# Performance work log

Measured on AMD Instinct MI355X. Metric: run time of the kernel, lower is better.

## Reference

```python
import jax, jax.numpy as jnp
import numpy as np

N, E, F_IN, HID, HEADS, NT, B = 50000, 400000, 32, 64, 4, 20, 64
IN1 = F_IN + HID  # 96, conv1 input dim after concat with node-type embedding


def _glorot(key, shape):
    fan_in = shape[0]
    return jax.random.normal(key, shape, dtype=jnp.float32) / np.sqrt(fan_in)


def setup_inputs() -> dict:
    key = jax.random.key(0)
    ks = jax.random.split(key, 40)
    inp = {
        "x": jax.random.normal(ks[0], (N, F_IN), dtype=jnp.float32),
        "edge_index": jax.random.randint(ks[1], (2, E), 0, N, dtype=jnp.int32),
        "edge_attr": jax.random.normal(ks[2], (E,), dtype=jnp.float32),
        "batch": jnp.sort(jax.random.randint(ks[3], (N,), 0, B, dtype=jnp.int32)),
        "node_type": jax.random.randint(ks[4], (N,), 0, NT, dtype=jnp.int32),
        # parameters
        "node_emb": jax.random.normal(ks[5], (NT, HID), dtype=jnp.float32) * 0.1,
        "edge_W": _glorot(ks[6], (1, HID)), "edge_b": jnp.zeros((HID,), jnp.float32),
        # GATConv 1 (in=96, out=64, heads=4, edge_dim=64, concat=False)
        "W1": _glorot(ks[7], (IN1, HEADS * HID)),
        "att_src1": jax.random.normal(ks[8], (HEADS, HID), jnp.float32) * 0.1,
        "att_dst1": jax.random.normal(ks[9], (HEADS, HID), jnp.float32) * 0.1,
        "We1": _glorot(ks[10], (HID, HEADS * HID)),
        "att_e1": jax.random.normal(ks[11], (HEADS, HID), jnp.float32) * 0.1,
        "b1": jnp.zeros((HID,), jnp.float32),
        # GATConv 2 (in=64)
        "W2": _glorot(ks[12], (HID, HEADS * HID)),
        "att_src2": jax.random.normal(ks[13], (HEADS, HID), jnp.float32) * 0.1,
        "att_dst2": jax.random.normal(ks[14], (HEADS, HID), jnp.float32) * 0.1,
        "We2": _glorot(ks[15], (HID, HEADS * HID)),
        "att_e2": jax.random.normal(ks[16], (HEADS, HID), jnp.float32) * 0.1,
        "b2": jnp.zeros((HID,), jnp.float32),
        # SAGEConv (mean aggr): out = mean_agg @ Wl + x @ Wr + b
        "sage_Wl": _glorot(ks[17], (HID, HID)), "sage_Wr": _glorot(ks[18], (HID, HID)),
        "sage_b": jnp.zeros((HID,), jnp.float32),
        "lin1_W": _glorot(ks[19], (HID, HID)), "lin1_b": jnp.zeros((HID,), jnp.float32),
        "lin2_W": _glorot(ks[20], (HID, HID)), "lin2_b": jnp.zeros((HID,), jnp.float32),
        "tel_W": _glorot(ks[21], (HID, 1)), "tel_b": jnp.zeros((1,), jnp.float32),
        "comp_W": _glorot(ks[22], (HID, 1)), "comp_b": jnp.zeros((1,), jnp.float32),
        "pch_W": _glorot(ks[23], (HID, 1)), "pch_b": jnp.zeros((1,), jnp.float32),
    }
    return inp


def _gat(x, src, dst, edge_h, W, att_s, att_d, We, att_e, b):
    n = x.shape[0]
    h = (x @ W).reshape(n, HEADS, HID)                       # [N,H,C]
    a_s = (h * att_s).sum(-1)                                # [N,H]
    a_d = (h * att_d).sum(-1)
    e = (edge_h @ We).reshape(-1, HEADS, HID)                # [E,H,C]
    a_e = (e * att_e).sum(-1)                                # [E,H]
    alpha = jax.nn.leaky_relu(a_s[src] + a_d[dst] + a_e, 0.2)
    m = jax.ops.segment_max(alpha, dst, num_segments=n)
    m = jnp.where(jnp.isfinite(m), m, 0.0)
    ex = jnp.exp(alpha - m[dst])
    den = jax.ops.segment_sum(ex, dst, num_segments=n)
    alpha = ex / (den[dst] + 1e-16)                          # segment softmax per dst
    out = jax.ops.segment_sum(h[src] * alpha[..., None], dst, num_segments=n)
    return out.mean(axis=1) + b                              # concat=False -> head mean


def reference(x, edge_index, edge_attr, batch, node_type, node_emb, edge_W, edge_b,
              W1, att_src1, att_dst1, We1, att_e1, b1,
              W2, att_src2, att_dst2, We2, att_e2, b2,
              sage_Wl, sage_Wr, sage_b, lin1_W, lin1_b, lin2_W, lin2_b,
              tel_W, tel_b, comp_W, comp_b, pch_W, pch_b):
    src, dst = edge_index[0], edge_index[1]
    edge_h = edge_attr[:, None] @ edge_W + edge_b            # [E,HID]
    h = jnp.concatenate([x, node_emb[node_type]], axis=-1)   # [N,96]
    h = jax.nn.elu(_gat(h, src, dst, edge_h, W1, att_src1, att_dst1, We1, att_e1, b1))
    h = jax.nn.elu(_gat(h, src, dst, edge_h, W2, att_src2, att_dst2, We2, att_e2, b2))
    # SAGEConv with mean aggregation
    deg = jax.ops.segment_sum(jnp.ones((src.shape[0],), h.dtype), dst, num_segments=N)
    agg = jax.ops.segment_sum(h[src], dst, num_segments=N) / jnp.maximum(deg, 1.0)[:, None]
    h = jax.nn.elu(agg @ sage_Wl + h @ sage_Wr + sage_b)
    # global mean pool over graphs
    cnt = jax.ops.segment_sum(jnp.ones((N,), h.dtype), batch, num_segments=B)
    g = jax.ops.segment_sum(h, batch, num_segments=B) / jnp.maximum(cnt, 1.0)[:, None]
    g = jax.nn.elu(g @ lin1_W + lin1_b)                      # dropout is identity in eval
    g = g @ lin2_W + lin2_b
    return (g @ tel_W + tel_b, g @ comp_W + comp_b, g @ pch_W + pch_b)
```

## Files before the change

kernel.cpp:

```cpp
#include <hip/hip_runtime.h>
#include <hip/hip_bf16.h>


#define NN 50000
#define NE 400000
#define FIN 32
#define NBATCH 64

typedef __hip_bfloat16 bf16;

__device__ __forceinline__ float b2f(bf16 v) { return __bfloat162float(v); }
__device__ __forceinline__ float lrelu(float x) { return x > 0.f ? x : 0.2f * x; }
__device__ __forceinline__ float eluf(float x) { return x > 0.f ? x : (expf(x) - 1.f); }

__device__ __forceinline__ float4 f4fma(float s, float4 w, float4 c) {
  c.x = fmaf(s, w.x, c.x); c.y = fmaf(s, w.y, c.y);
  c.z = fmaf(s, w.z, c.z); c.w = fmaf(s, w.w, c.w);
  return c;
}

__device__ __forceinline__ float4 upk4(uint2 u) {
  float4 f;
  f.x = __uint_as_float(u.x << 16);
  f.y = __uint_as_float(u.x & 0xffff0000u);
  f.z = __uint_as_float(u.y << 16);
  f.w = __uint_as_float(u.y & 0xffff0000u);
  return f;
}

__device__ __forceinline__ unsigned short bfbits(float f) {
  bf16 b = __float2bfloat16(f);
  unsigned short u;
  __builtin_memcpy(&u, &b, 2);
  return u;
}

__global__ __launch_bounds__(256) void k_pq(
    const float* __restrict__ We1, const float* __restrict__ atte1,
    const float* __restrict__ We2, const float* __restrict__ atte2,
    const float* __restrict__ edgeW, const float* __restrict__ edgeB,
    float* __restrict__ pq) {
  int t = threadIdx.x, h = t >> 6, c = t & 63;
  float sW1 = 0.f, sB1 = 0.f, sW2 = 0.f, sB2 = 0.f;
  for (int j = 0; j < 64; ++j) {
    float w = edgeW[j], b = edgeB[j];
    float we1 = We1[j * 256 + h * 64 + c];
    float we2 = We2[j * 256 + h * 64 + c];
    sW1 += w * we1; sB1 += b * we1;
    sW2 += w * we2; sB2 += b * we2;
  }
  float a1 = atte1[h * 64 + c], a2 = atte2[h * 64 + c];
  float p1 = sW1 * a1, q1 = sB1 * a1, p2 = sW2 * a2, q2 = sB2 * a2;
  for (int o = 32; o; o >>= 1) {
    p1 += __shfl_xor(p1, o); q1 += __shfl_xor(q1, o);
    p2 += __shfl_xor(p2, o); q2 += __shfl_xor(q2, o);
  }
  if (c == 0) { pq[h] = p1; pq[4 + h] = q1; pq[8 + h] = p2; pq[12 + h] = q2; }
}

__global__ void k_hist(const int* __restrict__ dst, int* __restrict__ cnt) {
  int e = blockIdx.x * 256 + threadIdx.x;
  if (e < NE) atomicAdd(&cnt[dst[e]], 1);
}

__global__ __launch_bounds__(1024) void k_scan(const int* __restrict__ cnt,
                                               int* __restrict__ off) {
  __shared__ int wsum[16];
  __shared__ int carry;
  int t = threadIdx.x, lane = t & 63, w = t >> 6;
  if (t == 0) { carry = 0; off[0] = 0; }
  __syncthreads();
  for (int base = 0; base < NN; base += 1024) {
    int idx = base + t;
    int v = (idx < NN) ? cnt[idx] : 0;
    int s = v;
    for (int o = 1; o < 64; o <<= 1) { int u = __shfl_up(s, o); if (lane >= o) s += u; }
    if (lane == 63) wsum[w] = s;
    __syncthreads();
    if (t < 16) {
      int ws = wsum[t];
      for (int o = 1; o < 16; o <<= 1) { int u = __shfl_up(ws, o); if (t >= o) ws += u; }
      wsum[t] = ws;
    }
    __syncthreads();
    int add = carry + (w ? wsum[w - 1] : 0);
    if (idx < NN) off[idx + 1] = add + s;
    __syncthreads();
    if (t == 0) carry += wsum[15];
    __syncthreads();
  }
}

__global__ void k_scatter(const int* __restrict__ src, const int* __restrict__ dst,
                          const float* __restrict__ ea, const int* __restrict__ off,
                          int* __restrict__ cur, int* __restrict__ csr_src,
                          float* __restrict__ csr_ea) {
  int e = blockIdx.x * 256 + threadIdx.x;
  if (e >= NE) return;
  int d = dst[e];
  int slot = off[d] + atomicAdd(&cur[d], 1);
  csr_src[slot] = src[e];
  csr_ea[slot] = ea[e];
}

template <int K, bool CONCAT>
__global__ __launch_bounds__(256) void k_gemm_att(
    const float* __restrict__ x, const int* __restrict__ ntype,
    const float* __restrict__ emb, const float* __restrict__ Ain,
    const float* __restrict__ W, const float* __restrict__ atts,
    const float* __restrict__ attd, bf16* __restrict__ hmat,
    float* __restrict__ as_, float* __restrict__ ad_) {
  __shared__ float Wl[K * 128];
  __shared__ float Ar[32 * K];
  int t = threadIdx.x;
  int ct = t & 31;
  int rg = t >> 5;
  int half = blockIdx.x & 1;
  for (int i = t; i < K * 128; i += 256)
    Wl[i] = W[(i >> 7) * 256 + half * 128 + (i & 127)];
  int gcol = half * 128 + ct * 4;
  float4 vsv = *reinterpret_cast<const float4*>(&atts[gcol]);
  float4 vdv = *reinterpret_cast<const float4*>(&attd[gcol]);
  const int NT = (NN + 31) / 32;
  const int NU = NT * 2;
  for (int u = blockIdx.x; u < NU; u += gridDim.x) {
    int r0 = (u >> 1) * 32;
    for (int i = t; i < 32 * K; i += 256) {
      int r = i / K, k = i - r * K;
      int n = r0 + r;
      float v = 0.f;
      if (n < NN) {
        if constexpr (CONCAT)
          v = (k < FIN) ? x[n * FIN + k] : emb[ntype[n] * 64 + (k - FIN)];
        else
          v = Ain[(size_t)n * K + k];
      }
      Ar[i] = v;
    }
    __syncthreads();
    float4 c0 = {0.f, 0.f, 0.f, 0.f}, c1 = c0, c2 = c0, c3 = c0;
    const float* Arow = &Ar[rg * 4 * K];
    #pragma unroll 4
    for (int k = 0; k < K; k += 4) {
      float4 w0 = *reinterpret_cast<const float4*>(&Wl[(k + 0) * 128 + ct * 4]);
      float4 w1 = *reinterpret_cast<const float4*>(&Wl[(k + 1) * 128 + ct * 4]);
      float4 w2 = *reinterpret_cast<const float4*>(&Wl[(k + 2) * 128 + ct * 4]);
      float4 w3 = *reinterpret_cast<const float4*>(&Wl[(k + 3) * 128 + ct * 4]);
      float4 a0 = *reinterpret_cast<const float4*>(&Arow[0 * K + k]);
      float4 a1 = *reinterpret_cast<const float4*>(&Arow[1 * K + k]);
      float4 a2 = *reinterpret_cast<const float4*>(&Arow[2 * K + k]);
      float4 a3 = *reinterpret_cast<const float4*>(&Arow[3 * K + k]);
      c0 = f4fma(a0.x, w0, c0); c0 = f4fma(a0.y, w1, c0);
      c0 = f4fma(a0.z, w2, c0); c0 = f4fma(a0.w, w3, c0);
      c1 = f4fma(a1.x, w0, c1); c1 = f4fma(a1.y, w1, c1);
      c1 = f4fma(a1.z, w2, c1); c1 = f4fma(a1.w, w3, c1);
      c2 = f4fma(a2.x, w0, c2); c2 = f4fma(a2.y, w1, c2);
      c2 = f4fma(a2.z, w2, c2); c2 = f4fma(a2.w, w3, c2);
      c3 = f4fma(a3.x, w0, c3); c3 = f4fma(a3.y, w1, c3);
      c3 = f4fma(a3.z, w2, c3); c3 = f4fma(a3.w, w3, c3);
    }
    int rb = r0 + rg * 4;
    float s0 = c0.x * vsv.x + c0.y * vsv.y + c0.z * vsv.z + c0.w * vsv.w;
    float s1 = c1.x * vsv.x + c1.y * vsv.y + c1.z * vsv.z + c1.w * vsv.w;
    float s2 = c2.x * vsv.x + c2.y * vsv.y + c2.z * vsv.z + c2.w * vsv.w;
    float s3 = c3.x * vsv.x + c3.y * vsv.y + c3.z * vsv.z + c3.w * vsv.w;
    float d0 = c0.x * vdv.x + c0.y * vdv.y + c0.z * vdv.z + c0.w * vdv.w;
    float d1 = c1.x * vdv.x + c1.y * vdv.y + c1.z * vdv.z + c1.w * vdv.w;
    float d2 = c2.x * vdv.x + c2.y * vdv.y + c2.z * vdv.z + c2.w * vdv.w;
    float d3 = c3.x * vdv.x + c3.y * vdv.y + c3.z * vdv.z + c3.w * vdv.w;
    ushort4 pk;
    if (rb + 0 < NN) {
      pk.x = bfbits(c0.x); pk.y = bfbits(c0.y); pk.z = bfbits(c0.z); pk.w = bfbits(c0.w);
      *reinterpret_cast<ushort4*>(&hmat[(size_t)(rb + 0) * 256 + gcol]) = pk;
    }
    if (rb + 1 < NN) {
      pk.x = bfbits(c1.x); pk.y = bfbits(c1.y); pk.z = bfbits(c1.z); pk.w = bfbits(c1.w);
      *reinterpret_cast<ushort4*>(&hmat[(size_t)(rb + 1) * 256 + gcol]) = pk;
    }
    if (rb + 2 < NN) {
      pk.x = bfbits(c2.x); pk.y = bfbits(c2.y); pk.z = bfbits(c2.z); pk.w = bfbits(c2.w);
      *reinterpret_cast<ushort4*>(&hmat[(size_t)(rb + 2) * 256 + gcol]) = pk;
    }
    if (rb + 3 < NN) {
      pk.x = bfbits(c3.x); pk.y = bfbits(c3.y); pk.z = bfbits(c3.z); pk.w = bfbits(c3.w);
      *reinterpret_cast<ushort4*>(&hmat[(size_t)(rb + 3) * 256 + gcol]) = pk;
    }
    for (int o = 1; o < 16; o <<= 1) {
      s0 += __shfl_xor(s0, o); s1 += __shfl_xor(s1, o);
      s2 += __shfl_xor(s2, o); s3 += __shfl_xor(s3, o);
      d0 += __shfl_xor(d0, o); d1 += __shfl_xor(d1, o);
      d2 += __shfl_xor(d2, o); d3 += __shfl_xor(d3, o);
    }
    if ((t & 15) == 0) {
      int h = half * 2 + ((t >> 4) & 1);
      if (rb + 0 < NN) { as_[(rb + 0) * 4 + h] = s0; ad_[(rb + 0) * 4 + h] = d0; }
      if (rb + 1 < NN) { as_[(rb + 1) * 4 + h] = s1; ad_[(rb + 1) * 4 + h] = d1; }
      if (rb + 2 < NN) { as_[(rb + 2) * 4 + h] = s2; ad_[(rb + 2) * 4 + h] = d2; }
      if (rb + 3 < NN) { as_[(rb + 3) * 4 + h] = s3; ad_[(rb + 3) * 4 + h] = d3; }
    }
    __syncthreads();
  }
}

__global__ __launch_bounds__(256) void k_gat(
    const int* __restrict__ off, const int* __restrict__ csr_src,
    const float* __restrict__ csr_ea, const float* __restrict__ as_,
    const float* __restrict__ ad_, const float* __restrict__ pq, int pqo,
    const bf16* __restrict__ hmat, const float* __restrict__ bias,
    float* __restrict__ out) {
  __shared__ float wlds[4][256];
  int wv = threadIdx.x >> 6;
  int wid = (blockIdx.x << 2) + wv;
  int lane = threadIdx.x & 63;
  if (wid >= NN) return;
  int beg = off[wid], end = off[wid + 1];
  int deg = end - beg;
  int hsel = lane >> 4;
  float4 D = reinterpret_cast<const float4*>(ad_)[wid];
  float p0 = pq[pqo + 0], p1 = pq[pqo + 1], p2 = pq[pqo + 2], p3 = pq[pqo + 3];
  float q0 = pq[pqo + 4], q1 = pq[pqo + 5], q2 = pq[pqo + 6], q3 = pq[pqo + 7];
  float4 acc = {0.f, 0.f, 0.f, 0.f};

  if (deg <= 64) {
    bool valid = lane < deg;
    float lx = -INFINITY, ly = -INFINITY, lz = -INFINITY, lw = -INFINITY;
    if (valid) {
      int s = csr_src[beg + lane];
      float ea = csr_ea[beg + lane];
      float4 A = reinterpret_cast<const float4*>(as_)[s];
      lx = lrelu(A.x + D.x + ea * p0 + q0);
      ly = lrelu(A.y + D.y + ea * p1 + q1);
      lz = lrelu(A.z + D.z + ea * p2 + q2);
      lw = lrelu(A.w + D.w + ea * p3 + q3);
    }
    float m0 = lx, m1 = ly, m2 = lz, m3 = lw;
    for (int o = 32; o; o >>= 1) {
      m0 = fmaxf(m0, __shfl_xor(m0, o));
      m1 = fmaxf(m1, __shfl_xor(m1, o));
      m2 = fmaxf(m2, __shfl_xor(m2, o));
      m3 = fmaxf(m3, __shfl_xor(m3, o));
    }
    float w0 = valid ? __expf(lx - m0) : 0.f;
    float w1 = valid ? __expf(ly - m1) : 0.f;
    float w2 = valid ? __expf(lz - m2) : 0.f;
    float w3 = valid ? __expf(lw - m3) : 0.f;
    float s0 = w0, s1 = w1, s2 = w2, s3 = w3;
    for (int o = 32; o; o >>= 1) {
      s0 += __shfl_xor(s0, o); s1 += __shfl_xor(s1, o);
      s2 += __shfl_xor(s2, o); s3 += __shfl_xor(s3, o);
    }
    float4 wv4;
    wv4.x = w0 / (s0 + 1e-16f);
    wv4.y = w1 / (s1 + 1e-16f);
    wv4.z = w2 / (s2 + 1e-16f);
    wv4.w = w3 / (s3 + 1e-16f);
    reinterpret_cast<float4*>(&wlds[wv][0])[lane] = wv4;
    const float* wp = &wlds[wv][0];
    int j = 0;
    for (; j + 4 <= deg; j += 4) {
      int sA = csr_src[beg + j + 0];
      int sB = csr_src[beg + j + 1];
      int sC = csr_src[beg + j + 2];
      int sD = csr_src[beg + j + 3];
      float wA = wp[4 * (j + 0) + hsel];
      float wB = wp[4 * (j + 1) + hsel];
      float wC = wp[4 * (j + 2) + hsel];
      float wD = wp[4 * (j + 3) + hsel];
      uint2 uA = *reinterpret_cast<const uint2*>(&hmat[(size_t)sA * 256 + 4 * lane]);
      uint2 uB = *reinterpret_cast<const uint2*>(&hmat[(size_t)sB * 256 + 4 * lane]);
      uint2 uC = *reinterpret_cast<const uint2*>(&hmat[(size_t)sC * 256 + 4 * lane]);
      uint2 uD = *reinterpret_cast<const uint2*>(&hmat[(size_t)sD * 256 + 4 * lane]);
      acc = f4fma(wA, upk4(uA), acc);
      acc = f4fma(wB, upk4(uB), acc);
      acc = f4fma(wC, upk4(uC), acc);
      acc = f4fma(wD, upk4(uD), acc);
    }
    for (; j < deg; ++j) {
      int s = csr_src[beg + j];
      float w = wp[4 * j + hsel];
      uint2 u = *reinterpret_cast<const uint2*>(&hmat[(size_t)s * 256 + 4 * lane]);
      acc = f4fma(w, upk4(u), acc);
    }
  } else {
    float m0 = -INFINITY, m1 = -INFINITY, m2 = -INFINITY, m3 = -INFINITY;
    float s0 = 0.f, s1 = 0.f, s2 = 0.f, s3 = 0.f;
    for (int e = beg + lane; e < end; e += 64) {
      int s = csr_src[e];
      float ea = csr_ea[e];
      float4 A = reinterpret_cast<const float4*>(as_)[s];
      float lx = lrelu(A.x + D.x + ea * p0 + q0);
      float ly = lrelu(A.y + D.y + ea * p1 + q1);
      float lz = lrelu(A.z + D.z + ea * p2 + q2);
      float lw = lrelu(A.w + D.w + ea * p3 + q3);
      float nm;
      nm = fmaxf(m0, lx); s0 = s0 * __expf(m0 - nm) + __expf(lx - nm); m0 = nm;
      nm = fmaxf(m1, ly); s1 = s1 * __expf(m1 - nm) + __expf(ly - nm); m1 = nm;
      nm = fmaxf(m2, lz); s2 = s2 * __expf(m2 - nm) + __expf(lz - nm); m2 = nm;
      nm = fmaxf(m3, lw); s3 = s3 * __expf(m3 - nm) + __expf(lw - nm); m3 = nm;
    }
    for (int o = 32; o; o >>= 1) {
      float om, os, nm;
      om = __shfl_xor(m0, o); os = __shfl_xor(s0, o); nm = fmaxf(m0, om);
      s0 = s0 * __expf(fmaxf(m0 - nm, -80.f)) + os * __expf(fmaxf(om - nm, -80.f)); m0 = nm;
      om = __shfl_xor(m1, o); os = __shfl_xor(s1, o); nm = fmaxf(m1, om);
      s1 = s1 * __expf(fmaxf(m1 - nm, -80.f)) + os * __expf(fmaxf(om - nm, -80.f)); m1 = nm;
      om = __shfl_xor(m2, o); os = __shfl_xor(s2, o); nm = fmaxf(m2, om);
      s2 = s2 * __expf(fmaxf(m2 - nm, -80.f)) + os * __expf(fmaxf(om - nm, -80.f)); m2 = nm;
      om = __shfl_xor(m3, o); os = __shfl_xor(s3, o); nm = fmaxf(m3, om);
      s3 = s3 * __expf(fmaxf(m3 - nm, -80.f)) + os * __expf(fmaxf(om - nm, -80.f)); m3 = nm;
    }
    float i0 = 1.f / (s0 + 1e-16f), i1 = 1.f / (s1 + 1e-16f);
    float i2 = 1.f / (s2 + 1e-16f), i3 = 1.f / (s3 + 1e-16f);
    float Dh = hsel == 0 ? D.x : hsel == 1 ? D.y : hsel == 2 ? D.z : D.w;
    float ph = hsel == 0 ? p0 : hsel == 1 ? p1 : hsel == 2 ? p2 : p3;
    float qh = hsel == 0 ? q0 : hsel == 1 ? q1 : hsel == 2 ? q2 : q3;
    float mh = hsel == 0 ? m0 : hsel == 1 ? m1 : hsel == 2 ? m2 : m3;
    float ih = hsel == 0 ? i0 : hsel == 1 ? i1 : hsel == 2 ? i2 : i3;
    for (int j = beg; j < end; ++j) {
      int s = csr_src[j];
      float ea = csr_ea[j];
      float4 A = reinterpret_cast<const float4*>(as_)[s];
      float Ah = hsel == 0 ? A.x : hsel == 1 ? A.y : hsel == 2 ? A.z : A.w;
      float l = lrelu(Ah + Dh + ea * ph + qh);
      float w = __expf(l - mh) * ih;
      uint2 u = *reinterpret_cast<const uint2*>(&hmat[(size_t)s * 256 + 4 * lane]);
      acc = f4fma(w, upk4(u), acc);
    }
  }
  acc.x += __shfl_xor(acc.x, 16); acc.y += __shfl_xor(acc.y, 16);
  acc.z += __shfl_xor(acc.z, 16); acc.w += __shfl_xor(acc.w, 16);
  acc.x += __shfl_xor(acc.x, 32); acc.y += __shfl_xor(acc.y, 32);
  acc.z += __shfl_xor(acc.z, 32); acc.w += __shfl_xor(acc.w, 32);
  if (lane < 16) {
    float4 bv = reinterpret_cast<const float4*>(bias)[lane];
    float4 r;
    r.x = eluf(0.25f * acc.x + bv.x);
    r.y = eluf(0.25f * acc.y + bv.y);
    r.z = eluf(0.25f * acc.z + bv.z);
    r.w = eluf(0.25f * acc.w + bv.w);
    reinterpret_cast<float4*>(&out[(size_t)wid * 64])[lane] = r;
  }
}

__global__ __launch_bounds__(256) void k_agg(
    const int* __restrict__ off, const int* __restrict__ csr_src,
    const float* __restrict__ h3, float* __restrict__ agg) {
  int wid = (blockIdx.x << 2) + (threadIdx.x >> 6);
  int lane = threadIdx.x & 63;
  if (wid >= NN) return;
  int beg = off[wid], end = off[wid + 1];
  float acc = 0.f;
  int e = beg;
  for (; e + 4 <= end; e += 4) {
    int s0 = csr_src[e + 0], s1 = csr_src[e + 1];
    int s2 = csr_src[e + 2], s3 = csr_src[e + 3];
    float v0 = h3[(size_t)s0 * 64 + lane];
    float v1 = h3[(size_t)s1 * 64 + lane];
    float v2 = h3[(size_t)s2 * 64 + lane];
    float v3 = h3[(size_t)s3 * 64 + lane];
    acc += (v0 + v1) + (v2 + v3);
  }
  for (; e < end; ++e) acc += h3[(size_t)csr_src[e] * 64 + lane];
  agg[(size_t)wid * 64 + lane] = acc / fmaxf((float)(end - beg), 1.f);
}

__global__ __launch_bounds__(256) void k_sage_mm(
    const float* __restrict__ agg, const float* __restrict__ h3,
    const float* __restrict__ Wl, const float* __restrict__ Wr,
    const float* __restrict__ bias, float* __restrict__ out) {
  __shared__ float WlS[4096];
  __shared__ float WrS[4096];
  __shared__ float Ag[2048];
  __shared__ float Hr[2048];
  int t = threadIdx.x;
  for (int i = t; i < 4096; i += 256) { WlS[i] = Wl[i]; WrS[i] = Wr[i]; }
  int ct = t & 15, rg = t >> 4;
  float4 bv = reinterpret_cast<const float4*>(bias)[ct];
  for (int r0 = blockIdx.x * 32; r0 < NN; r0 += gridDim.x * 32) {
    for (int i = t; i < 2048; i += 256) {
      int n = r0 + (i >> 6);
      float va = 0.f, vh = 0.f;
      if (n < NN) {
        va = agg[(size_t)n * 64 + (i & 63)];
        vh = h3[(size_t)n * 64 + (i & 63)];
      }
      Ag[i] = va; Hr[i] = vh;
    }
    __syncthreads();
    float4 c0 = {0.f, 0.f, 0.f, 0.f}, c1 = c0;
    const float* a0 = &Ag[(rg * 2 + 0) * 64];
    const float* a1 = &Ag[(rg * 2 + 1) * 64];
    const float* h0 = &Hr[(rg * 2 + 0) * 64];
    const float* h1 = &Hr[(rg * 2 + 1) * 64];
    #pragma unroll 4
    for (int k = 0; k < 64; k += 4) {
      float4 wl0 = *reinterpret_cast<const float4*>(&WlS[(k + 0) * 64 + ct * 4]);
      float4 wl1 = *reinterpret_cast<const float4*>(&WlS[(k + 1) * 64 + ct * 4]);
      float4 wl2 = *reinterpret_cast<const float4*>(&WlS[(k + 2) * 64 + ct * 4]);
      float4 wl3 = *reinterpret_cast<const float4*>(&WlS[(k + 3) * 64 + ct * 4]);
      float4 wr0 = *reinterpret_cast<const float4*>(&WrS[(k + 0) * 64 + ct * 4]);
      float4 wr1 = *reinterpret_cast<const float4*>(&WrS[(k + 1) * 64 + ct * 4]);
      float4 wr2 = *reinterpret_cast<const float4*>(&WrS[(k + 2) * 64 + ct * 4]);
      float4 wr3 = *reinterpret_cast<const float4*>(&WrS[(k + 3) * 64 + ct * 4]);
      float4 aa0 = *reinterpret_cast<const float4*>(&a0[k]);
      float4 aa1 = *reinterpret_cast<const float4*>(&a1[k]);
      float4 hh0 = *reinterpret_cast<const float4*>(&h0[k]);
      float4 hh1 = *reinterpret_cast<const float4*>(&h1[k]);
      c0 = f4fma(aa0.x, wl0, c0); c0 = f4fma(aa0.y, wl1, c0);
      c0 = f4fma(aa0.z, wl2, c0); c0 = f4fma(aa0.w, wl3, c0);
      c0 = f4fma(hh0.x, wr0, c0); c0 = f4fma(hh0.y, wr1, c0);
      c0 = f4fma(hh0.z, wr2, c0); c0 = f4fma(hh0.w, wr3, c0);
      c1 = f4fma(aa1.x, wl0, c1); c1 = f4fma(aa1.y, wl1, c1);
      c1 = f4fma(aa1.z, wl2, c1); c1 = f4fma(aa1.w, wl3, c1);
      c1 = f4fma(hh1.x, wr0, c1); c1 = f4fma(hh1.y, wr1, c1);
      c1 = f4fma(hh1.z, wr2, c1); c1 = f4fma(hh1.w, wr3, c1);
    }
    int n0 = r0 + rg * 2;
    if (n0 + 0 < NN) {
      float4 r;
      r.x = eluf(c0.x + bv.x); r.y = eluf(c0.y + bv.y);
      r.z = eluf(c0.z + bv.z); r.w = eluf(c0.w + bv.w);
      *reinterpret_cast<float4*>(&out[(size_t)(n0 + 0) * 64 + ct * 4]) = r;
    }
    if (n0 + 1 < NN) {
      float4 r;
      r.x = eluf(c1.x + bv.x); r.y = eluf(c1.y + bv.y);
      r.z = eluf(c1.z + bv.z); r.w = eluf(c1.w + bv.w);
      *reinterpret_cast<float4*>(&out[(size_t)(n0 + 1) * 64 + ct * 4]) = r;
    }
    __syncthreads();
  }
}

__device__ __forceinline__ int lowerb(const int* __restrict__ a, int n, int key) {
  int lo = 0, hi = n;
  while (lo < hi) { int mid = (lo + hi) >> 1; if (a[mid] < key) lo = mid + 1; else hi = mid; }
  return lo;
}

__global__ __launch_bounds__(256) void k_pool(const float* __restrict__ hs,
                                              const int* __restrict__ batch,
                                              float* __restrict__ g) {
  int b = blockIdx.x;
  int lo = lowerb(batch, NN, b), hi = lowerb(batch, NN, b + 1);
  int t = threadIdx.x, lane = t & 63, w = t >> 6;
  float acc = 0.f;
  for (int n = lo + w; n < hi; n += 4) acc += hs[(size_t)n * 64 + lane];
  __shared__ float red[4][64];
  red[w][lane] = acc;
  __syncthreads();
  if (w == 0) {
    float v = red[0][lane] + red[1][lane] + red[2][lane] + red[3][lane];
    g[b * 64 + lane] = v / fmaxf((float)(hi - lo), 1.f);
  }
}

__global__ __launch_bounds__(256) void k_head(
    const float* __restrict__ g, const float* __restrict__ l1W,
    const float* __restrict__ l1b, const float* __restrict__ l2W,
    const float* __restrict__ l2b, const float* __restrict__ telW,
    const float* __restrict__ telb, const float* __restrict__ compW,
    const float* __restrict__ compb, const float* __restrict__ pchW,
    const float* __restrict__ pchb, float* __restrict__ out) {
  __shared__ float gS[4096];
  __shared__ float WS[4096];
  __shared__ float hS[4096];
  int t = threadIdx.x;
  for (int i = t; i < 4096; i += 256) { gS[i] = g[i]; WS[i] = l1W[i]; }
  __syncthreads();
  for (int i = t; i < 4096; i += 256) {
    int r = i >> 6, j = i & 63;
    float s = 0.f;
    for (int k = 0; k < 64; ++k) s += gS[r * 64 + k] * WS[k * 64 + j];
    hS[i] = eluf(s + l1b[j]);
  }
  __syncthreads();
  for (int i = t; i < 4096; i += 256) WS[i] = l2W[i];
  __syncthreads();
  for (int i = t; i < 4096; i += 256) {
    int r = i >> 6, j = i & 63;
    float s = 0.f;
    for (int k = 0; k < 64; ++k) s += hS[r * 64 + k] * WS[k * 64 + j];
    gS[i] = s + l2b[j];
  }
  __syncthreads();
  if (t < 192) {
    int head = t >> 6, r = t & 63;
    const float* Wv = head == 0 ? telW : (head == 1 ? compW : pchW);
    float bb = head == 0 ? telb[0] : (head == 1 ? compb[0] : pchb[0]);
    float s = 0.f;
    for (int k = 0; k < 64; ++k) s += gS[r * 64 + k] * Wv[k];
    out[t] = s + bb;
  }
}

extern "C" void kernel_launch(void* const* d_in, const int* in_sizes, int n_in,
                              void* d_out, int out_size, void* d_ws, size_t ws_size,
                              hipStream_t stream) {
  const float* x     = (const float*)d_in[0];
  const int*   eidx  = (const int*)d_in[1];
  const float* eattr = (const float*)d_in[2];
  const int*   batch = (const int*)d_in[3];
  const int*   ntype = (const int*)d_in[4];
  const float* nemb  = (const float*)d_in[5];
  const float* edgeW = (const float*)d_in[6];
  const float* edgeB = (const float*)d_in[7];
  const float* W1    = (const float*)d_in[8];
  const float* atts1 = (const float*)d_in[9];
  const float* attd1 = (const float*)d_in[10];
  const float* We1   = (const float*)d_in[11];
  const float* atte1 = (const float*)d_in[12];
  const float* b1    = (const float*)d_in[13];
  const float* W2    = (const float*)d_in[14];
  const float* atts2 = (const float*)d_in[15];
  const float* attd2 = (const float*)d_in[16];
  const float* We2   = (const float*)d_in[17];
  const float* atte2 = (const float*)d_in[18];
  const float* b2    = (const float*)d_in[19];
  const float* sageWl = (const float*)d_in[20];
  const float* sageWr = (const float*)d_in[21];
  const float* sageB  = (const float*)d_in[22];
  const float* l1W = (const float*)d_in[23];
  const float* l1b = (const float*)d_in[24];
  const float* l2W = (const float*)d_in[25];
  const float* l2b = (const float*)d_in[26];
  const float* telW  = (const float*)d_in[27];
  const float* telb  = (const float*)d_in[28];
  const float* compW = (const float*)d_in[29];
  const float* compb = (const float*)d_in[30];
  const float* pchW  = (const float*)d_in[31];
  const float* pchb  = (const float*)d_in[32];

  char* wp = (char*)d_ws;
  auto alloc = [&](size_t bytes) -> char* {
    char* p = wp;
    wp += (bytes + 255) & ~(size_t)255;
    return p;
  };
  float*  pq      = (float*)alloc(16 * 4);
  int*    cnt     = (int*)alloc((size_t)NN * 4);
  int*    off     = (int*)alloc(((size_t)NN + 1) * 4);
  int*    csr_src = (int*)alloc((size_t)NE * 4);
  float*  csr_ea  = (float*)alloc((size_t)NE * 4);
  float*  as_     = (float*)alloc((size_t)NN * 16);
  float*  ad_     = (float*)alloc((size_t)NN * 16);
  bf16*   hmat    = (bf16*)alloc((size_t)NN * 256 * 2);
  float*  nodeA   = (float*)alloc((size_t)NN * 64 * 4);
  float*  nodeB   = (float*)alloc((size_t)NN * 64 * 4);
  float*  aggbuf  = (float*)alloc((size_t)NN * 64 * 4);
  float*  gbuf    = (float*)alloc(64 * 64 * 4);

  const int* srcI = eidx;
  const int* dstI = eidx + NE;

  hipMemsetAsync(cnt, 0, (size_t)NN * 4, stream);
  k_pq<<<1, 256, 0, stream>>>(We1, atte1, We2, atte2, edgeW, edgeB, pq);
  k_hist<<<(NE + 255) / 256, 256, 0, stream>>>(dstI, cnt);
  k_scan<<<1, 1024, 0, stream>>>(cnt, off);
  hipMemsetAsync(cnt, 0, (size_t)NN * 4, stream);
  k_scatter<<<(NE + 255) / 256, 256, 0, stream>>>(srcI, dstI, eattr, off, cnt,
                                                  csr_src, csr_ea);
  k_gemm_att<96, true><<<1024, 256, 0, stream>>>(
      x, ntype, nemb, nullptr, W1, atts1, attd1, hmat, as_, ad_);
  k_gat<<<NN / 4, 256, 0, stream>>>(off, csr_src, csr_ea, as_, ad_, pq, 0,
                                    hmat, b1, nodeA);
  k_gemm_att<64, false><<<1024, 256, 0, stream>>>(
      nullptr, nullptr, nullptr, nodeA, W2, atts2, attd2, hmat, as_, ad_);
  k_gat<<<NN / 4, 256, 0, stream>>>(off, csr_src, csr_ea, as_, ad_, pq, 8,
                                    hmat, b2, nodeB);
  k_agg<<<NN / 4, 256, 0, stream>>>(off, csr_src, nodeB, aggbuf);
  k_sage_mm<<<1024, 256, 0, stream>>>(aggbuf, nodeB, sageWl, sageWr, sageB,
                                      nodeA);
  k_pool<<<NBATCH, 256, 0, stream>>>(nodeA, batch, gbuf);
  k_head<<<1, 256, 0, stream>>>(gbuf, l1W, l1b, l2W, l2b, telW, telb, compW,
                                compb, pchW, pchb, (float*)d_out);
}
```

Measured before the change: 543.7 us.

## Use split-bf16 MFMA for GAT linear projections with fused attention dots

Replaces the FP32 FMA GEMM for both GAT layer projections with MFMA bf16 16x16x32 instructions. Near-FP32 accuracy is kept by splitting each operand into high and low bf16 parts and summing three products. New kernels pre-split the weights and the concatenated layer-1 input, and the first GAT kernel now writes its output directly as hi/lo bf16 pairs for layer 2. This trades extra split kernels and more memory traffic (two bf16 copies of A, read straight from global without LDS) for matrix-core throughput.

```diff
diff --git a/kernel.cpp b/kernel.cpp
--- a/kernel.cpp
+++ b/kernel.cpp
@@ -8,6 +8,8 @@
 #define NBATCH 64
 
 typedef __hip_bfloat16 bf16;
+typedef short bf16x8 __attribute__((ext_vector_type(8)));
+typedef float f32x4 __attribute__((ext_vector_type(4)));
 
 __device__ __forceinline__ float b2f(bf16 v) { return __bfloat162float(v); }
 __device__ __forceinline__ float lrelu(float x) { return x > 0.f ? x : 0.2f * x; }
@@ -33,6 +35,9 @@
   unsigned short u;
   __builtin_memcpy(&u, &b, 2);
   return u;
+}
+__device__ __forceinline__ float hi_f(unsigned short u) {
+  return __uint_as_float((unsigned int)u << 16);
 }
 
 __global__ __launch_bounds__(256) void k_pq(
@@ -103,102 +108,108 @@
   csr_ea[slot] = ea[e];
 }
 
-template <int K, bool CONCAT>
-__global__ __launch_bounds__(256) void k_gemm_att(
+__global__ __launch_bounds__(256) void k_splitA(
     const float* __restrict__ x, const int* __restrict__ ntype,
-    const float* __restrict__ emb, const float* __restrict__ Ain,
-    const float* __restrict__ W, const float* __restrict__ atts,
-    const float* __restrict__ attd, bf16* __restrict__ hmat,
-    float* __restrict__ as_, float* __restrict__ ad_) {
-  __shared__ float Wl[K * 128];
-  __shared__ float Ar[32 * K];
-  int t = threadIdx.x;
-  int ct = t & 31;
-  int rg = t >> 5;
-  int half = blockIdx.x & 1;
-  for (int i = t; i < K * 128; i += 256)
-    Wl[i] = W[(i >> 7) * 256 + half * 128 + (i & 127)];
-  int gcol = half * 128 + ct * 4;
-  float4 vsv = *reinterpret_cast<const float4*>(&atts[gcol]);
-  float4 vdv = *reinterpret_cast<const float4*>(&attd[gcol]);
-  const int NT = (NN + 31) / 32;
-  const int NU = NT * 2;
-  for (int u = blockIdx.x; u < NU; u += gridDim.x) {
-    int r0 = (u >> 1) * 32;
-    for (int i = t; i < 32 * K; i += 256) {
-      int r = i / K, k = i - r * K;
-      int n = r0 + r;
-      float v = 0.f;
-      if (n < NN) {
-        if constexpr (CONCAT)
-          v = (k < FIN) ? x[n * FIN + k] : emb[ntype[n] * 64 + (k - FIN)];
-        else
-          v = Ain[(size_t)n * K + k];
+    const float* __restrict__ emb, unsigned short* __restrict__ Ah,
+    unsigned short* __restrict__ Al) {
+  const int total = NN * 96;
+  for (int i = blockIdx.x * 256 + threadIdx.x; i < total; i += gridDim.x * 256) {
+    int n = i / 96, k = i - n * 96;
+    float v = (k < FIN) ? x[n * FIN + k] : emb[ntype[n] * 64 + (k - FIN)];
+    unsigned short h = bfbits(v);
+    Ah[i] = h;
+    Al[i] = bfbits(v - hi_f(h));
+  }
+}
+
+__global__ __launch_bounds__(256) void k_splitW(
+    const float* __restrict__ W1, const float* __restrict__ W2,
+    unsigned short* __restrict__ B1h, unsigned short* __restrict__ B1l,
+    unsigned short* __restrict__ B2h, unsigned short* __restrict__ B2l) {
+  int t = blockIdx.x * 256 + threadIdx.x;
+  if (t < 256 * 96) {
+    int n = t / 96, k = t - n * 96;
+    float v = W1[k * 256 + n];
+    unsigned short h = bfbits(v);
+    B1h[t] = h; B1l[t] = bfbits(v - hi_f(h));
+  }
+  if (t < 256 * 64) {
+    int n = t >> 6, k = t & 63;
+    float v = W2[k * 256 + n];
+    unsigned short h = bfbits(v);
+    B2h[t] = h; B2l[t] = bfbits(v - hi_f(h));
+  }
+}
+
+template <int K>
+__global__ __launch_bounds__(256) void k_mm_mfma(
+    const unsigned short* __restrict__ Ah, const unsigned short* __restrict__ Al,
+    const unsigned short* __restrict__ Bh, const unsigned short* __restrict__ Bl,
+    const float* __restrict__ atts, const float* __restrict__ attd,
+    bf16* __restrict__ hmat, float* __restrict__ as_, float* __restrict__ ad_) {
+  int m0 = blockIdx.x * 64;
+  int w = threadIdx.x >> 6;
+  int lane = threadIdx.x & 63;
+  int lr = lane & 15;
+  int lc = lane >> 4;
+  float attsv[4], attdv[4];
+  #pragma unroll
+  for (int nt = 0; nt < 4; ++nt) {
+    attsv[nt] = atts[w * 64 + nt * 16 + lr];
+    attdv[nt] = attd[w * 64 + nt * 16 + lr];
+  }
+  f32x4 acc[4][4] = {};
+  #pragma unroll
+  for (int ks = 0; ks < K; ks += 32) {
+    int koff = ks + lc * 8;
+    bf16x8 ah[4], al[4], bh[4], bl[4];
+    #pragma unroll
+    for (int mt = 0; mt < 4; ++mt) {
+      int m = m0 + mt * 16 + lr;
+      if (m > NN - 1) m = NN - 1;
+      ah[mt] = *reinterpret_cast<const bf16x8*>(&Ah[(size_t)m * K + koff]);
+      al[mt] = *reinterpret_cast<const bf16x8*>(&Al[(size_t)m * K + koff]);
+    }
+    #pragma unroll
+    for (int nt = 0; nt < 4; ++nt) {
+      int n = w * 64 + nt * 16 + lr;
+      bh[nt] = *reinterpret_cast<const bf16x8*>(&Bh[(size_t)n * K + koff]);
+      bl[nt] = *reinterpret_cast<const bf16x8*>(&Bl[(size_t)n * K + koff]);
+    }
+    #pragma unroll
+    for (int mt = 0; mt < 4; ++mt) {
+      #pragma unroll
+      for (int nt = 0; nt < 4; ++nt) {
+        acc[mt][nt] = __builtin_amdgcn_mfma_f32_16x16x32_bf16(ah[mt], bh[nt], acc[mt][nt], 0, 0, 0);
+        acc[mt][nt] = __builtin_amdgcn_mfma_f32_16x16x32_bf16(al[mt], bh[nt], acc[mt][nt], 0, 0, 0);
+        acc[mt][nt] = __builtin_amdgcn_mfma_f32_16x16x32_bf16(ah[mt], bl[nt], acc[mt][nt], 0, 0, 0);
       }
-      Ar[i] = v;
-    }
-    __syncthreads();
-    float4 c0 = {0.f, 0.f, 0.f, 0.f}, c1 = c0, c2 = c0, c3 = c0;
-    const float* Arow = &Ar[rg * 4 * K];
-    #pragma unroll 4
-    for (int k = 0; k < K; k += 4) {
-      float4 w0 = *reinterpret_cast<const float4*>(&Wl[(k + 0) * 128 + ct * 4]);
-      float4 w1 = *reinterpret_cast<const float4*>(&Wl[(k + 1) * 128 + ct * 4]);
-      float4 w2 = *reinterpret_cast<const float4*>(&Wl[(k + 2) * 128 + ct * 4]);
-      float4 w3 = *reinterpret_cast<const float4*>(&Wl[(k + 3) * 128 + ct * 4]);
-      float4 a0 = *reinterpret_cast<const float4*>(&Arow[0 * K + k]);
-      float4 a1 = *reinterpret_cast<const float4*>(&Arow[1 * K + k]);
-      float4 a2 = *reinterpret_cast<const float4*>(&Arow[2 * K + k]);
-      float4 a3 = *reinterpret_cast<const float4*>(&Arow[3 * K + k]);
-      c0 = f4fma(a0.x, w0, c0); c0 = f4fma(a0.y, w1, c0);
-      c0 = f4fma(a0.z, w2, c0); c0 = f4fma(a0.w, w3, c0);
-      c1 = f4fma(a1.x, w0, c1); c1 = f4fma(a1.y, w1, c1);
-      c1 = f4fma(a1.z, w2, c1); c1 = f4fma(a1.w, w3, c1);
-      c2 = f4fma(a2.x, w0, c2); c2 = f4fma(a2.y, w1, c2);
-      c2 = f4fma(a2.z, w2, c2); c2 = f4fma(a2.w, w3, c2);
-      c3 = f4fma(a3.x, w0, c3); c3 = f4fma(a3.y, w1, c3);
-      c3 = f4fma(a3.z, w2, c3); c3 = f4fma(a3.w, w3, c3);
-    }
-    int rb = r0 + rg * 4;
-    float s0 = c0.x * vsv.x + c0.y * vsv.y + c0.z * vsv.z + c0.w * vsv.w;
-    float s1 = c1.x * vsv.x + c1.y * vsv.y + c1.z * vsv.z + c1.w * vsv.w;
-    float s2 = c2.x * vsv.x + c2.y * vsv.y + c2.z * vsv.z + c2.w * vsv.w;
-    float s3 = c3.x * vsv.x + c3.y * vsv.y + c3.z * vsv.z + c3.w * vsv.w;
-    float d0 = c0.x * vdv.x + c0.y * vdv.y + c0.z * vdv.z + c0.w * vdv.w;
-    float d1 = c1.x * vdv.x + c1.y * vdv.y + c1.z * vdv.z + c1.w * vdv.w;
-    float d2 = c2.x * vdv.x + c2.y * vdv.y + c2.z * vdv.z + c2.w * vdv.w;
-    float d3 = c3.x * vdv.x + c3.y * vdv.y + c3.z * vdv.z + c3.w * vdv.w;
-    ushort4 pk;
-    if (rb + 0 < NN) {
-      pk.x = bfbits(c0.x); pk.y = bfbits(c0.y); pk.z = bfbits(c0.z); pk.w = bfbits(c0.w);
-      *reinterpret_cast<ushort4*>(&hmat[(size_t)(rb + 0) * 256 + gcol]) = pk;
-    }
-    if (rb + 1 < NN) {
-      pk.x = bfbits(c1.x); pk.y = bfbits(c1.y); pk.z = bfbits(c1.z); pk.w = bfbits(c1.w);
-      *reinterpret_cast<ushort4*>(&hmat[(size_t)(rb + 1) * 256 + gcol]) = pk;
-    }
-    if (rb + 2 < NN) {
-      pk.x = bfbits(c2.x); pk.y = bfbits(c2.y); pk.z = bfbits(c2.z); pk.w = bfbits(c2.w);
-      *reinterpret_cast<ushort4*>(&hmat[(size_t)(rb + 2) * 256 + gcol]) = pk;
-    }
-    if (rb + 3 < NN) {
-      pk.x = bfbits(c3.x); pk.y = bfbits(c3.y); pk.z = bfbits(c3.z); pk.w = bfbits(c3.w);
-      *reinterpret_cast<ushort4*>(&hmat[(size_t)(rb + 3) * 256 + gcol]) = pk;
-    }
-    for (int o = 1; o < 16; o <<= 1) {
-      s0 += __shfl_xor(s0, o); s1 += __shfl_xor(s1, o);
-      s2 += __shfl_xor(s2, o); s3 += __shfl_xor(s3, o);
-      d0 += __shfl_xor(d0, o); d1 += __shfl_xor(d1, o);
-      d2 += __shfl_xor(d2, o); d3 += __shfl_xor(d3, o);
-    }
-    if ((t & 15) == 0) {
-      int h = half * 2 + ((t >> 4) & 1);
-      if (rb + 0 < NN) { as_[(rb + 0) * 4 + h] = s0; ad_[(rb + 0) * 4 + h] = d0; }
-      if (rb + 1 < NN) { as_[(rb + 1) * 4 + h] = s1; ad_[(rb + 1) * 4 + h] = d1; }
-      if (rb + 2 < NN) { as_[(rb + 2) * 4 + h] = s2; ad_[(rb + 2) * 4 + h] = d2; }
-      if (rb + 3 < NN) { as_[(rb + 3) * 4 + h] = s3; ad_[(rb + 3) * 4 + h] = d3; }
-    }
-    __syncthreads();
+    }
+  }
+  #pragma unroll
+  for (int mt = 0; mt < 4; ++mt) {
+    #pragma unroll
+    for (int reg = 0; reg < 4; ++reg) {
+      int row = m0 + mt * 16 + lc * 4 + reg;
+      float sS = 0.f, sD = 0.f;
+      #pragma unroll
+      for (int nt = 0; nt < 4; ++nt) {
+        float v = acc[mt][nt][reg];
+        sS += v * attsv[nt];
+        sD += v * attdv[nt];
+      }
+      for (int o = 1; o < 16; o <<= 1) {
+        sS += __shfl_xor(sS, o);
+        sD += __shfl_xor(sD, o);
+      }
+      if (row < NN) {
+        #pragma unroll
+        for (int nt = 0; nt < 4; ++nt)
+          hmat[(size_t)row * 256 + w * 64 + nt * 16 + lr] =
+              __float2bfloat16(acc[mt][nt][reg]);
+        if (lr == 0) { as_[row * 4 + w] = sS; ad_[row * 4 + w] = sD; }
+      }
+    }
   }
 }
 
@@ -207,7 +218,8 @@
     const float* __restrict__ csr_ea, const float* __restrict__ as_,
     const float* __restrict__ ad_, const float* __restrict__ pq, int pqo,
     const bf16* __restrict__ hmat, const float* __restrict__ bias,
-    float* __restrict__ out) {
+    float* __restrict__ outf, unsigned short* __restrict__ oph,
+    unsigned short* __restrict__ opl) {
   __shared__ float wlds[4][256];
   int wv = threadIdx.x >> 6;
   int wid = (blockIdx.x << 2) + wv;
@@ -338,7 +350,16 @@
     r.y = eluf(0.25f * acc.y + bv.y);
     r.z = eluf(0.25f * acc.z + bv.z);
     r.w = eluf(0.25f * acc.w + bv.w);
-    reinterpret_cast<float4*>(&out[(size_t)wid * 64])[lane] = r;
+    if (outf) reinterpret_cast<float4*>(&outf[(size_t)wid * 64])[lane] = r;
+    if (oph) {
+      ushort4 h4, l4;
+      h4.x = bfbits(r.x); l4.x = bfbits(r.x - hi_f(h4.x));
+      h4.y = bfbits(r.y); l4.y = bfbits(r.y - hi_f(h4.y));
+      h4.z = bfbits(r.z); l4.z = bfbits(r.z - hi_f(h4.z));
+      h4.w = bfbits(r.w); l4.w = bfbits(r.w - hi_f(h4.w));
+      *reinterpret_cast<ushort4*>(&oph[(size_t)wid * 64 + lane * 4]) = h4;
+      *reinterpret_cast<ushort4*>(&opl[(size_t)wid * 64 + lane * 4]) = l4;
+    }
   }
 }
 
@@ -545,10 +566,19 @@
   float*  as_     = (float*)alloc((size_t)NN * 16);
   float*  ad_     = (float*)alloc((size_t)NN * 16);
   bf16*   hmat    = (bf16*)alloc((size_t)NN * 256 * 2);
-  float*  nodeA   = (float*)alloc((size_t)NN * 64 * 4);
   float*  nodeB   = (float*)alloc((size_t)NN * 64 * 4);
   float*  aggbuf  = (float*)alloc((size_t)NN * 64 * 4);
-  float*  gbuf    = (float*)alloc(64 * 64 * 4);
+  unsigned short* B1h = (unsigned short*)alloc(256 * 96 * 2);
+  unsigned short* B1l = (unsigned short*)alloc(256 * 96 * 2);
+  unsigned short* B2h = (unsigned short*)alloc(256 * 64 * 2);
+  unsigned short* B2l = (unsigned short*)alloc(256 * 64 * 2);
+  char* R = alloc((size_t)NN * 96 * 2 * 2);
+  unsigned short* A1h = (unsigned short*)R;
+  unsigned short* A1l = A1h + (size_t)NN * 96;
+  unsigned short* A2h = (unsigned short*)R;
+  unsigned short* A2l = A2h + (size_t)NN * 64;
+  float* sageout = (float*)R;
+  float* gbuf = (float*)alloc(64 * 64 * 4);
 
   const int* srcI = eidx;
   const int* dstI = eidx + NE;
@@ -560,18 +590,20 @@
   hipMemsetAsync(cnt, 0, (size_t)NN * 4, stream);
   k_scatter<<<(NE + 255) / 256, 256, 0, stream>>>(srcI, dstI, eattr, off, cnt,
                                                   csr_src, csr_ea);
-  k_gemm_att<96, true><<<1024, 256, 0, stream>>>(
-      x, ntype, nemb, nullptr, W1, atts1, attd1, hmat, as_, ad_);
+  k_splitW<<<96, 256, 0, stream>>>(W1, W2, B1h, B1l, B2h, B2l);
+  k_splitA<<<2048, 256, 0, stream>>>(x, ntype, nemb, A1h, A1l);
+  k_mm_mfma<96><<<(NN + 63) / 64, 256, 0, stream>>>(
+      A1h, A1l, B1h, B1l, atts1, attd1, hmat, as_, ad_);
   k_gat<<<NN / 4, 256, 0, stream>>>(off, csr_src, csr_ea, as_, ad_, pq, 0,
-                                    hmat, b1, nodeA);
-  k_gemm_att<64, false><<<1024, 256, 0, stream>>>(
-      nullptr, nullptr, nullptr, nodeA, W2, atts2, attd2, hmat, as_, ad_);
+                                    hmat, b1, nullptr, A2h, A2l);
+  k_mm_mfma<64><<<(NN + 63) / 64, 256, 0, stream>>>(
+      A2h, A2l, B2h, B2l, atts2, attd2, hmat, as_, ad_);
   k_gat<<<NN / 4, 256, 0, stream>>>(off, csr_src, csr_ea, as_, ad_, pq, 8,
-                                    hmat, b2, nodeB);
+                                    hmat, b2, nodeB, nullptr, nullptr);
   k_agg<<<NN / 4, 256, 0, stream>>>(off, csr_src, nodeB, aggbuf);
   k_sage_mm<<<1024, 256, 0, stream>>>(aggbuf, nodeB, sageWl, sageWr, sageB,
-                                      nodeA);
-  k_pool<<<NBATCH, 256, 0, stream>>>(nodeA, batch, gbuf);
+                                      sageout);
+  k_pool<<<NBATCH, 256, 0, stream>>>(sageout, batch, gbuf);
   k_head<<<1, 256, 0, stream>>>(gbuf, l1W, l1b, l2W, l2b, telW, telb, compW,
                                 compb, pchW, pchb, (float*)d_out);
 }
```

New measurement: 490.3 us. 1.11x faster.
